# Performance work log

Hardware: AMD Instinct MI355X
Metric: run time of the kernel (lower is better)

The kernel has to match this reference:

```python
import jax, jax.numpy as jnp
import numpy as np

B, T, C = 4, 2048, 1024
N_HEADS = 16
HEAD_DIM = C // N_HEADS


def setup_inputs() -> dict:
    key = jax.random.key(0)
    k1, k2, k3 = jax.random.split(key, 3)
    x = jax.random.normal(k1, (B, T, C), dtype=jnp.float32)
    # torch Linear weights stored as [out, in]; we store as [in, out] for x @ W
    w_qkv = jax.random.normal(k2, (C, 3 * C), dtype=jnp.float32) * (1.0 / np.sqrt(C))
    w_proj = jax.random.normal(k3, (C, C), dtype=jnp.float32) * (1.0 / np.sqrt(C))
    return {"x": x, "w_qkv": w_qkv, "w_proj": w_proj}


def reference(x, w_qkv, w_proj):
    Bx, Tx, Cx = x.shape
    qkv = x @ w_qkv                               # [B,T,3C]
    q, k, v = jnp.split(qkv, 3, axis=-1)

    def to_heads(t):
        return t.reshape(Bx, Tx, N_HEADS, HEAD_DIM).transpose(0, 2, 1, 3)  # [B,H,T,D]

    q, k, v = to_heads(q), to_heads(k), to_heads(v)
    scale = 1.0 / np.sqrt(HEAD_DIM).astype(np.float32)
    scores = jnp.einsum('bhqd,bhkd->bhqk', q, k) * scale  # [B,H,T,T]
    causal = jnp.tril(jnp.ones((Tx, Tx), dtype=bool))
    scores = jnp.where(causal[None, None, :, :], scores, -jnp.inf)
    weights = jax.nn.softmax(scores, axis=-1)
    out = jnp.einsum('bhqk,bhkd->bhqd', weights, v)       # [B,H,T,D]
    out = out.transpose(0, 2, 1, 3).reshape(Bx, Tx, Cx)   # [B,T,C]
    return out @ w_proj
```

## Files before the change

### kernel.cpp

```cpp
#include <hip/hip_runtime.h>
#include <hip/hip_bf16.h>

typedef unsigned short u16;
typedef unsigned int u32;
typedef __attribute__((ext_vector_type(8))) __bf16 bf16x8;
typedef __attribute__((ext_vector_type(4))) float f32x4;
typedef __attribute__((ext_vector_type(4))) short short4v;
typedef __attribute__((ext_vector_type(2))) u32 u32x2;

#define B_ 4
#define T_ 2048
#define C_ 1024
#define NH_ 16
#define HD_ 64

static __device__ __forceinline__ u16 f2bf(float f) {
  u32 u = __builtin_bit_cast(u32, f);
  u32 r = (u + 0x7fffu + ((u >> 16) & 1u)) >> 16;
  return (u16)r;
}

static __device__ __forceinline__ u32 pack2bf(float a, float b) {
  u32 ua = __builtin_bit_cast(u32, a) + 0x8000u;
  u32 ub = __builtin_bit_cast(u32, b) + 0x8000u;
  return __builtin_amdgcn_perm(ub, ua, 0x07060302u);
}

static __device__ __forceinline__ float fexp2(float x) {
#if __has_builtin(__builtin_amdgcn_exp2f)
  return __builtin_amdgcn_exp2f(x);
#else
  return exp2f(x);
#endif
}

static __device__ __forceinline__ void load_lds16(const u16* g, u16* l) {
  __builtin_amdgcn_global_load_lds(
      (const __attribute__((address_space(1))) u32*)g,
      (__attribute__((address_space(3))) u32*)l, 16, 0, 0);
}

static __device__ __forceinline__ f32x4 mfma32(bf16x8 a, bf16x8 b, f32x4 c) {
  return __builtin_amdgcn_mfma_f32_16x16x32_bf16(a, b, c, 0, 0, 0);
}

static __device__ __forceinline__ f32x4 mfma16(short4v a, short4v b, f32x4 c) {
#if __has_builtin(__builtin_amdgcn_mfma_f32_16x16x16bf16_1k)
  return __builtin_amdgcn_mfma_f32_16x16x16bf16_1k(a, b, c, 0, 0, 0);
#else
  asm volatile("v_mfma_f32_16x16x16_bf16 %0, %1, %2, %0\n\t"
               "s_nop 7\n\ts_nop 7"
               : "+v"(c)
               : "v"(a), "v"(b));
  return c;
#endif
}

__global__ __launch_bounds__(256) void cast_bf(const float* __restrict__ in,
                                               u16* __restrict__ out, int n) {
  int i = (blockIdx.x * 256 + threadIdx.x) * 8;
  if (i >= n) return;
  float4 a = *(const float4*)(in + i);
  float4 b = *(const float4*)(in + i + 4);
  u16 r[8] = {f2bf(a.x), f2bf(a.y), f2bf(a.z), f2bf(a.w),
              f2bf(b.x), f2bf(b.y), f2bf(b.z), f2bf(b.w)};
  *(uint4*)(out + i) = *(const uint4*)r;
}

__global__ __launch_bounds__(256) void transpose_cast(const float* __restrict__ in,
                                                      u16* __restrict__ out,
                                                      int K, int N) {
  __shared__ float tile[32][33];
  int bx = blockIdx.x * 32;
  int by = blockIdx.y * 32;
  int tx = threadIdx.x & 31, ty = threadIdx.x >> 5;
  for (int r = ty; r < 32; r += 8)
    tile[r][tx] = in[(size_t)(by + r) * N + bx + tx];
  __syncthreads();
  for (int r = ty; r < 32; r += 8)
    out[(size_t)(bx + r) * K + by + tx] = f2bf(tile[tx][r]);
}

template <bool STORE_BF16, bool SCALE_Q>
__global__ __launch_bounds__(256) void gemm_bt(const u16* __restrict__ A,
                                               const u16* __restrict__ Bt,
                                               void* __restrict__ Cv,
                                               int M, int N, int K,
                                               float qscale) {
  __shared__ __align__(16) u16 As[128 * 64];
  __shared__ __align__(16) u16 Bs[128 * 64];
  const int tid = threadIdx.x;
  const int wave = tid >> 6, lane = tid & 63;
  const int wm = (wave >> 1) * 64, wn = (wave & 1) * 64;
  const int m0 = blockIdx.x * 128, n0 = blockIdx.y * 128;
  const int col = lane & 15, quad = lane >> 4;
  const int lcol = (lane & 7) * 8;
  const int sg = ((lane & 7) ^ ((lane >> 3) & 7)) * 8;
  const int ag = ((quad ^ (col & 7)) * 8);

  f32x4 acc[4][4] = {};

  for (int kt = 0; kt < K; kt += 64) {
    __syncthreads();
    for (int i = 0; i < 4; i++) {
      int row = (wave * 4 + i) * 8 + (lane >> 3);
      load_lds16(A + (size_t)(m0 + row) * K + kt + sg, &As[row * 64 + lcol]);
      load_lds16(Bt + (size_t)(n0 + row) * K + kt + sg, &Bs[row * 64 + lcol]);
    }
    __syncthreads();
    for (int ks = 0; ks < 64; ks += 32) {
      const int o = ag ^ ks;
      bf16x8 af[4], bfr[4];
      for (int t = 0; t < 4; t++) {
        af[t]  = *(const bf16x8*)(&As[(wm + t * 16 + col) * 64 + o]);
        bfr[t] = *(const bf16x8*)(&Bs[(wn + t * 16 + col) * 64 + o]);
      }
      for (int i = 0; i < 4; i++)
        for (int j = 0; j < 4; j++)
          acc[i][j] = mfma32(af[i], bfr[j], acc[i][j]);
    }
  }

  const int rbase = quad * 4;
  for (int i = 0; i < 4; i++)
    for (int j = 0; j < 4; j++) {
      int r = m0 + wm + i * 16 + rbase;
      int c = n0 + wn + j * 16 + col;
      float sc = (SCALE_Q && c < 1024) ? qscale : 1.0f;
      if (STORE_BF16) {
        for (int reg = 0; reg < 4; reg++)
          ((u16*)Cv)[(size_t)(r + reg) * N + c] = f2bf(acc[i][j][reg] * sc);
      } else {
        for (int reg = 0; reg < 4; reg++)
          ((float*)Cv)[(size_t)(r + reg) * N + c] = acc[i][j][reg];
      }
    }
}

__global__ __launch_bounds__(256) void v_permute(const u16* __restrict__ qkv,
                                                 u16* __restrict__ vt) {
  const int jt = blockIdx.x, bh = blockIdx.y, b = bh >> 4, h = bh & 15;
  __shared__ u16 tile[64][68];
  const int tid = threadIdx.x;
  {
    int tl = tid >> 2, c = (tid & 3) * 16;
    const u16* src = qkv + (size_t)(b * 2048 + jt * 64 + tl) * 3072 + 2048 + h * 64 + c;
    *(uint4*)(&tile[tl][c])     = *(const uint4*)(src);
    *(uint4*)(&tile[tl][c + 8]) = *(const uint4*)(src + 8);
  }
  __syncthreads();
  int d = tid >> 2, gq = tid & 3;
  u16 ob[16] __attribute__((aligned(16)));
  for (int j = 0; j < 16; j++) {
    int g = gq * 16 + j;
    int tl = (g & 3) | (((g >> 4) & 3) << 2) | (((g >> 2) & 3) << 4);
    ob[j] = tile[tl][d];
  }
  u16* dst = vt + ((size_t)bh * 64 + d) * 2048 + jt * 64 + gq * 16;
  *(uint4*)(dst) = *(const uint4*)ob;
  *(uint4*)(dst + 8) = *(const uint4*)(ob + 8);
}

__global__ __launch_bounds__(256, 4) void attn_fused(const u16* __restrict__ qkv,
                                                     const u16* __restrict__ vt,
                                                     u16* __restrict__ o) {
  const int i = blockIdx.x >> 6;
  const int bh = blockIdx.x & 63, b = bh >> 4, h = bh & 15;
  const int tid = threadIdx.x, wave = tid >> 6, lane = tid & 63;
  const int col = lane & 15, quad = lane >> 4;

  const int qt0 = i, qt1 = 31 - i;
  const int jtmax = qt1;

  __shared__ __align__(16) u16 Ks[2][4096];
  __shared__ __align__(16) u16 Vs[2][4096];

  const u16* qkb = qkv + (size_t)b * 2048 * 3072;
  const u16* vtb = vt + (size_t)bh * 64 * 2048;

  bf16x8 qf[2][2];
  for (int t = 0; t < 2; t++) {
    int q = (t ? qt1 : qt0) * 64 + wave * 16 + col;
    const u16* qp = qkb + (size_t)q * 3072 + h * 64;
    qf[t][0] = *(const bf16x8*)(qp + quad * 8);
    qf[t][1] = *(const bf16x8*)(qp + 32 + quad * 8);
  }

  f32x4 lacc[2] = {};
  f32x4 Oacc[2][4] = {};

  const int sg  = ((lane & 7) ^ ((lane >> 3) & 7)) * 8;
  const int swq = col & 7;
  const int kg0 = (quad ^ swq) * 8;
  const int vg0 = ((2 * quad) ^ swq) * 8;

  auto stage = [&](int jt, int buf) {
    for (int ii = 0; ii < 2; ii++) {
      int idx = (ii * 4 + wave) * 64 + lane;
      int r = idx >> 3;
      load_lds16(qkb + (size_t)(jt * 64 + r) * 3072 + 1024 + h * 64 + sg,
                 &Ks[buf][idx * 8]);
      load_lds16(vtb + (size_t)r * 2048 + jt * 64 + sg, &Vs[buf][idx * 8]);
    }
  };

  auto softmax_tile = [&](f32x4* s, int t, u32* pbt) {
    f32x4 ps = {};
    for (int nt = 0; nt < 4; nt++) {
      f32x4 p;
      for (int r = 0; r < 4; r++) p[r] = fexp2(s[nt][r]);
      ps += p;
      pbt[nt * 2]     = pack2bf(p[0], p[1]);
      pbt[nt * 2 + 1] = pack2bf(p[2], p[3]);
    }
    lacc[t] += ps;
  };

  stage(0, 0);
  for (int jt = 0; jt <= jtmax; jt++) {
    const int cur = jt & 1;
    __syncthreads();
    if (jt < jtmax) stage(jt + 1, cur ^ 1);

    const u16* K_ = Ks[cur];
    const u16* V_ = Vs[cur];
    const bool act0 = (jt <= qt0);

    f32x4 s0[4] = {}, s1[4] = {};
    for (int nt = 0; nt < 4; nt++) {
      bf16x8 k0 = *(const bf16x8*)(K_ + (nt * 16 + col) * 64 + kg0);
      bf16x8 k1 = *(const bf16x8*)(K_ + (nt * 16 + col) * 64 + (kg0 ^ 32));
      if (act0) {
        s0[nt] = mfma32(k0, qf[0][0], s0[nt]);
        s0[nt] = mfma32(k1, qf[0][1], s0[nt]);
      }
      s1[nt] = mfma32(k0, qf[1][0], s1[nt]);
      s1[nt] = mfma32(k1, qf[1][1], s1[nt]);
    }

    u32 pb0[8], pb1[8];
    if (act0) {
      if (jt == qt0) {
        for (int nt = 0; nt < 4; nt++)
          for (int r = 0; r < 4; r++) {
            int j = nt * 16 + quad * 4 + r, q = wave * 16 + col;
            if (j > q) s0[nt][r] = -INFINITY;
          }
      }
      softmax_tile(s0, 0, pb0);
    }
    if (jt == qt1) {
      for (int nt = 0; nt < 4; nt++)
        for (int r = 0; r < 4; r++) {
          int j = nt * 16 + quad * 4 + r, q = wave * 16 + col;
          if (j > q) s1[nt][r] = -INFINITY;
        }
    }
    softmax_tile(s1, 1, pb1);

    for (int dt = 0; dt < 4; dt++) {
      uint4 vb0 = *(const uint4*)(V_ + (dt * 16 + col) * 64 + vg0);
      uint4 vb1 = *(const uint4*)(V_ + (dt * 16 + col) * 64 + (vg0 ^ 8));
      short4v vf[4];
      vf[0] = __builtin_bit_cast(short4v, (u32x2){vb0.x, vb0.y});
      vf[1] = __builtin_bit_cast(short4v, (u32x2){vb0.z, vb0.w});
      vf[2] = __builtin_bit_cast(short4v, (u32x2){vb1.x, vb1.y});
      vf[3] = __builtin_bit_cast(short4v, (u32x2){vb1.z, vb1.w});
      for (int nt = 0; nt < 4; nt++) {
        if (act0) {
          short4v pf0 = __builtin_bit_cast(short4v, (u32x2){pb0[nt * 2], pb0[nt * 2 + 1]});
          Oacc[0][dt] = mfma16(vf[nt], pf0, Oacc[0][dt]);
        }
        short4v pf1 = __builtin_bit_cast(short4v, (u32x2){pb1[nt * 2], pb1[nt * 2 + 1]});
        Oacc[1][dt] = mfma16(vf[nt], pf1, Oacc[1][dt]);
      }
    }
  }

  for (int t = 0; t < 2; t++) {
    float l = (lacc[t][0] + lacc[t][1]) + (lacc[t][2] + lacc[t][3]);
    l += __shfl_xor(l, 16, 64);
    l += __shfl_xor(l, 32, 64);
    float rl = 1.0f / l;
    int q = (t ? qt1 : qt0) * 64 + wave * 16 + col;
    u16* op = o + (size_t)(b * 2048 + q) * 1024 + h * 64;
    for (int dt = 0; dt < 4; dt++) {
      u16 ob[4] __attribute__((aligned(8)));
      for (int r = 0; r < 4; r++) ob[r] = f2bf(Oacc[t][dt][r] * rl);
      *(uint2*)(op + dt * 16 + quad * 4) = *(const uint2*)ob;
    }
  }
}

extern "C" void kernel_launch(void* const* d_in, const int* in_sizes, int n_in,
                              void* d_out, int out_size, void* d_ws, size_t ws_size,
                              hipStream_t stream) {
  const float* x      = (const float*)d_in[0];
  const float* w_qkv  = (const float*)d_in[1];
  const float* w_proj = (const float*)d_in[2];
  float* out = (float*)d_out;

  u16* x_bf    = (u16*)d_ws;
  u16* wqkvT   = x_bf + (size_t)8192 * 1024;
  u16* wprojT  = wqkvT + (size_t)3072 * 1024;
  u16* qkv_bf  = wprojT + (size_t)1024 * 1024;
  u16* attn_bf = qkv_bf + (size_t)8192 * 3072;
  u16* vt_perm = x_bf;

  const float qscale = 0.125f * 1.44269504f;

  cast_bf<<<4096, 256, 0, stream>>>(x, x_bf, 8192 * 1024);
  transpose_cast<<<dim3(96, 32), 256, 0, stream>>>(w_qkv, wqkvT, 1024, 3072);
  transpose_cast<<<dim3(32, 32), 256, 0, stream>>>(w_proj, wprojT, 1024, 1024);

  gemm_bt<true, true><<<dim3(64, 24), 256, 0, stream>>>(
      x_bf, wqkvT, qkv_bf, 8192, 3072, 1024, qscale);

  v_permute<<<dim3(32, 64), 256, 0, stream>>>(qkv_bf, vt_perm);

  attn_fused<<<1024, 256, 0, stream>>>(qkv_bf, vt_perm, attn_bf);

  gemm_bt<false, false><<<dim3(64, 8), 256, 0, stream>>>(
      attn_bf, wprojT, out, 8192, 1024, 1024, 1.0f);
}
```

Before: 264.6 us.

## Fuse V transpose into QKV GEMM epilogue and merge prep kernels

```diff
diff --git a/kernel.cpp b/kernel.cpp
--- a/kernel.cpp
+++ b/kernel.cpp
@@ -4,6 +4,7 @@
 typedef unsigned short u16;
 typedef unsigned int u32;
 typedef __attribute__((ext_vector_type(8))) __bf16 bf16x8;
+typedef __attribute__((ext_vector_type(2))) __bf16 bf16x2;
 typedef __attribute__((ext_vector_type(4))) float f32x4;
 typedef __attribute__((ext_vector_type(4))) short short4v;
 typedef __attribute__((ext_vector_type(2))) u32 u32x2;
@@ -20,10 +21,15 @@
   return (u16)r;
 }
 
-static __device__ __forceinline__ u32 pack2bf(float a, float b) {
+static __device__ __forceinline__ u32 pk_bf16(float a, float b) {
+#if __has_builtin(__builtin_amdgcn_cvt_pk_bf16_f32)
+  bf16x2 v = __builtin_amdgcn_cvt_pk_bf16_f32(a, b);
+  return __builtin_bit_cast(u32, v);
+#else
   u32 ua = __builtin_bit_cast(u32, a) + 0x8000u;
   u32 ub = __builtin_bit_cast(u32, b) + 0x8000u;
   return __builtin_amdgcn_perm(ub, ua, 0x07060302u);
+#endif
 }
 
 static __device__ __forceinline__ float fexp2(float x) {
@@ -56,24 +62,36 @@
 #endif
 }
 
-__global__ __launch_bounds__(256) void cast_bf(const float* __restrict__ in,
-                                               u16* __restrict__ out, int n) {
-  int i = (blockIdx.x * 256 + threadIdx.x) * 8;
-  if (i >= n) return;
-  float4 a = *(const float4*)(in + i);
-  float4 b = *(const float4*)(in + i + 4);
-  u16 r[8] = {f2bf(a.x), f2bf(a.y), f2bf(a.z), f2bf(a.w),
-              f2bf(b.x), f2bf(b.y), f2bf(b.z), f2bf(b.w)};
-  *(uint4*)(out + i) = *(const uint4*)r;
-}
-
-__global__ __launch_bounds__(256) void transpose_cast(const float* __restrict__ in,
-                                                      u16* __restrict__ out,
-                                                      int K, int N) {
+__global__ __launch_bounds__(256) void prep(const float* __restrict__ x,
+                                            const float* __restrict__ wqkv,
+                                            const float* __restrict__ wproj,
+                                            u16* __restrict__ x_bf,
+                                            u16* __restrict__ wqkvT,
+                                            u16* __restrict__ wprojT) {
   __shared__ float tile[32][33];
-  int bx = blockIdx.x * 32;
-  int by = blockIdx.y * 32;
-  int tx = threadIdx.x & 31, ty = threadIdx.x >> 5;
+  const int bid = blockIdx.x, tid = threadIdx.x;
+  if (bid < 4096) {
+    int i = (bid * 256 + tid) * 8;
+    float4 a = *(const float4*)(x + i);
+    float4 b = *(const float4*)(x + i + 4);
+    u16 r[8] = {f2bf(a.x), f2bf(a.y), f2bf(a.z), f2bf(a.w),
+                f2bf(b.x), f2bf(b.y), f2bf(b.z), f2bf(b.w)};
+    *(uint4*)(x_bf + i) = *(const uint4*)r;
+    return;
+  }
+  const float* in;
+  u16* out;
+  int K = 1024, N, bx, by;
+  if (bid < 4096 + 3072) {
+    int id = bid - 4096;
+    in = wqkv; out = wqkvT; N = 3072;
+    bx = (id % 96) * 32; by = (id / 96) * 32;
+  } else {
+    int id = bid - 7168;
+    in = wproj; out = wprojT; N = 1024;
+    bx = (id % 32) * 32; by = (id / 32) * 32;
+  }
+  int tx = tid & 31, ty = tid >> 5;
   for (int r = ty; r < 32; r += 8)
     tile[r][tx] = in[(size_t)(by + r) * N + bx + tx];
   __syncthreads();
@@ -81,12 +99,84 @@
     out[(size_t)(bx + r) * K + by + tx] = f2bf(tile[tx][r]);
 }
 
-template <bool STORE_BF16, bool SCALE_Q>
-__global__ __launch_bounds__(256) void gemm_bt(const u16* __restrict__ A,
-                                               const u16* __restrict__ Bt,
-                                               void* __restrict__ Cv,
-                                               int M, int N, int K,
-                                               float qscale) {
+__global__ __launch_bounds__(256) void gemm_qkv(const u16* __restrict__ A,
+                                                const u16* __restrict__ Bt,
+                                                u16* __restrict__ qk,
+                                                u16* __restrict__ vt,
+                                                float qscale) {
+  const int K_ = 1024;
+  __shared__ __align__(16) u16 smem[128 * 136];
+  u16* As = smem;
+  u16* Bs = smem + 128 * 64;
+  const int tid = threadIdx.x;
+  const int wave = tid >> 6, lane = tid & 63;
+  const int wm = (wave >> 1) * 64, wn = (wave & 1) * 64;
+  const int m0 = blockIdx.x * 128, n0 = blockIdx.y * 128;
+  const int col = lane & 15, quad = lane >> 4;
+  const int lcol = (lane & 7) * 8;
+  const int sg = ((lane & 7) ^ ((lane >> 3) & 7)) * 8;
+  const int ag = ((quad ^ (col & 7)) * 8);
+
+  f32x4 acc[4][4] = {};
+
+  for (int kt = 0; kt < K_; kt += 64) {
+    __syncthreads();
+    for (int i = 0; i < 4; i++) {
+      int row = (wave * 4 + i) * 8 + (lane >> 3);
+      load_lds16(A + (size_t)(m0 + row) * K_ + kt + sg, &As[row * 64 + lcol]);
+      load_lds16(Bt + (size_t)(n0 + row) * K_ + kt + sg, &Bs[row * 64 + lcol]);
+    }
+    __syncthreads();
+    for (int ks = 0; ks < 64; ks += 32) {
+      const int o = ag ^ ks;
+      bf16x8 af[4], bfr[4];
+      for (int t = 0; t < 4; t++) {
+        af[t]  = *(const bf16x8*)(&As[(wm + t * 16 + col) * 64 + o]);
+        bfr[t] = *(const bf16x8*)(&Bs[(wn + t * 16 + col) * 64 + o]);
+      }
+      for (int i = 0; i < 4; i++)
+        for (int j = 0; j < 4; j++)
+          acc[i][j] = mfma32(af[i], bfr[j], acc[i][j]);
+    }
+  }
+
+  if (n0 < 2048) {
+    for (int i = 0; i < 4; i++)
+      for (int j = 0; j < 4; j++) {
+        int r = m0 + wm + i * 16 + quad * 4;
+        int c = n0 + wn + j * 16 + col;
+        float sc = (c < 1024) ? qscale : 1.0f;
+        for (int reg = 0; reg < 4; reg++)
+          qk[(size_t)(r + reg) * 2048 + c] = f2bf(acc[i][j][reg] * sc);
+      }
+    return;
+  }
+
+  __syncthreads();
+  for (int i = 0; i < 4; i++)
+    for (int j = 0; j < 4; j++) {
+      int cl = wn + j * 16 + col;
+      u16 tmp[4] __attribute__((aligned(8)));
+      for (int reg = 0; reg < 4; reg++) tmp[reg] = f2bf(acc[i][j][reg]);
+      *(unsigned long long*)(&smem[cl * 136 + wm + i * 4 + quad * 16]) =
+          *(const unsigned long long*)tmp;
+    }
+  __syncthreads();
+  {
+    int cl = tid >> 1, half = tid & 1;
+    int cv = (n0 - 2048) + cl, hh = cv >> 6, d = cv & 63;
+    int b = m0 >> 11;
+    u16* dst = vt + ((size_t)((b << 4) + hh) * 64 + d) * 2048 + (m0 & 2047) + half * 64;
+    const u16* src = &smem[cl * 136 + half * 64];
+    for (int ii = 0; ii < 8; ii++)
+      *(uint4*)(dst + ii * 8) = *(const uint4*)(src + ii * 8);
+  }
+}
+
+__global__ __launch_bounds__(256) void gemm_proj(const u16* __restrict__ A,
+                                                 const u16* __restrict__ Bt,
+                                                 float* __restrict__ C,
+                                                 int M, int N, int K) {
   __shared__ __align__(16) u16 As[128 * 64];
   __shared__ __align__(16) u16 Bs[128 * 64];
   const int tid = threadIdx.x;
@@ -121,47 +211,16 @@
     }
   }
 
-  const int rbase = quad * 4;
   for (int i = 0; i < 4; i++)
     for (int j = 0; j < 4; j++) {
-      int r = m0 + wm + i * 16 + rbase;
+      int r = m0 + wm + i * 16 + quad * 4;
       int c = n0 + wn + j * 16 + col;
-      float sc = (SCALE_Q && c < 1024) ? qscale : 1.0f;
-      if (STORE_BF16) {
-        for (int reg = 0; reg < 4; reg++)
-          ((u16*)Cv)[(size_t)(r + reg) * N + c] = f2bf(acc[i][j][reg] * sc);
-      } else {
-        for (int reg = 0; reg < 4; reg++)
-          ((float*)Cv)[(size_t)(r + reg) * N + c] = acc[i][j][reg];
-      }
-    }
-}
-
-__global__ __launch_bounds__(256) void v_permute(const u16* __restrict__ qkv,
-                                                 u16* __restrict__ vt) {
-  const int jt = blockIdx.x, bh = blockIdx.y, b = bh >> 4, h = bh & 15;
-  __shared__ u16 tile[64][68];
-  const int tid = threadIdx.x;
-  {
-    int tl = tid >> 2, c = (tid & 3) * 16;
-    const u16* src = qkv + (size_t)(b * 2048 + jt * 64 + tl) * 3072 + 2048 + h * 64 + c;
-    *(uint4*)(&tile[tl][c])     = *(const uint4*)(src);
-    *(uint4*)(&tile[tl][c + 8]) = *(const uint4*)(src + 8);
-  }
-  __syncthreads();
-  int d = tid >> 2, gq = tid & 3;
-  u16 ob[16] __attribute__((aligned(16)));
-  for (int j = 0; j < 16; j++) {
-    int g = gq * 16 + j;
-    int tl = (g & 3) | (((g >> 4) & 3) << 2) | (((g >> 2) & 3) << 4);
-    ob[j] = tile[tl][d];
-  }
-  u16* dst = vt + ((size_t)bh * 64 + d) * 2048 + jt * 64 + gq * 16;
-  *(uint4*)(dst) = *(const uint4*)ob;
-  *(uint4*)(dst + 8) = *(const uint4*)(ob + 8);
-}
-
-__global__ __launch_bounds__(256, 4) void attn_fused(const u16* __restrict__ qkv,
+      for (int reg = 0; reg < 4; reg++)
+        C[(size_t)(r + reg) * N + c] = acc[i][j][reg];
+    }
+}
+
+__global__ __launch_bounds__(256, 4) void attn_fused(const u16* __restrict__ qk,
                                                      const u16* __restrict__ vt,
                                                      u16* __restrict__ o) {
   const int i = blockIdx.x >> 6;
@@ -175,13 +234,13 @@
   __shared__ __align__(16) u16 Ks[2][4096];
   __shared__ __align__(16) u16 Vs[2][4096];
 
-  const u16* qkb = qkv + (size_t)b * 2048 * 3072;
+  const u16* qkb = qk + (size_t)b * 2048 * 2048;
   const u16* vtb = vt + (size_t)bh * 64 * 2048;
 
   bf16x8 qf[2][2];
   for (int t = 0; t < 2; t++) {
     int q = (t ? qt1 : qt0) * 64 + wave * 16 + col;
-    const u16* qp = qkb + (size_t)q * 3072 + h * 64;
+    const u16* qp = qkb + (size_t)q * 2048 + h * 64;
     qf[t][0] = *(const bf16x8*)(qp + quad * 8);
     qf[t][1] = *(const bf16x8*)(qp + 32 + quad * 8);
   }
@@ -194,14 +253,25 @@
   const int kg0 = (quad ^ swq) * 8;
   const int vg0 = ((2 * quad) ^ swq) * 8;
 
-  auto stage = [&](int jt, int buf) {
-    for (int ii = 0; ii < 2; ii++) {
-      int idx = (ii * 4 + wave) * 64 + lane;
-      int r = idx >> 3;
-      load_lds16(qkb + (size_t)(jt * 64 + r) * 3072 + 1024 + h * 64 + sg,
-                 &Ks[buf][idx * 8]);
-      load_lds16(vtb + (size_t)r * 2048 + jt * 64 + sg, &Vs[buf][idx * 8]);
-    }
+  const int r0 = wave * 8 + (lane >> 3);
+  const int r1 = r0 + 32;
+  const u16* kp0 = qkb + (size_t)r0 * 2048 + 1024 + h * 64 + sg;
+  const u16* kp1 = qkb + (size_t)r1 * 2048 + 1024 + h * 64 + sg;
+  const u16* vp0 = vtb + (size_t)r0 * 2048 + sg;
+  const u16* vp1 = vtb + (size_t)r1 * 2048 + sg;
+  u16* kd0 = &Ks[0][(wave * 64 + lane) * 8];
+  u16* kd1 = kd0 + 2048;
+  u16* vd0 = &Vs[0][(wave * 64 + lane) * 8];
+  u16* vd1 = vd0 + 2048;
+
+  auto stage = [&](int buf) {
+    int bo = buf * 4096;
+    load_lds16(kp0, kd0 + bo);
+    load_lds16(kp1, kd1 + bo);
+    load_lds16(vp0, vd0 + bo);
+    load_lds16(vp1, vd1 + bo);
+    kp0 += 64 * 2048; kp1 += 64 * 2048;
+    vp0 += 64; vp1 += 64;
   };
 
   auto softmax_tile = [&](f32x4* s, int t, u32* pbt) {
@@ -210,17 +280,17 @@
       f32x4 p;
       for (int r = 0; r < 4; r++) p[r] = fexp2(s[nt][r]);
       ps += p;
-      pbt[nt * 2]     = pack2bf(p[0], p[1]);
-      pbt[nt * 2 + 1] = pack2bf(p[2], p[3]);
+      pbt[nt * 2]     = pk_bf16(p[0], p[1]);
+      pbt[nt * 2 + 1] = pk_bf16(p[2], p[3]);
     }
     lacc[t] += ps;
   };
 
-  stage(0, 0);
+  stage(0);
   for (int jt = 0; jt <= jtmax; jt++) {
     const int cur = jt & 1;
     __syncthreads();
-    if (jt < jtmax) stage(jt + 1, cur ^ 1);
+    if (jt < jtmax) stage(cur ^ 1);
 
     const u16* K_ = Ks[cur];
     const u16* V_ = Vs[cur];
@@ -303,23 +373,17 @@
   u16* x_bf    = (u16*)d_ws;
   u16* wqkvT   = x_bf + (size_t)8192 * 1024;
   u16* wprojT  = wqkvT + (size_t)3072 * 1024;
-  u16* qkv_bf  = wprojT + (size_t)1024 * 1024;
-  u16* attn_bf = qkv_bf + (size_t)8192 * 3072;
-  u16* vt_perm = x_bf;
+  u16* qk_buf  = wprojT + (size_t)1024 * 1024;
+  u16* vt_perm = qk_buf + (size_t)8192 * 2048;
+  u16* attn_bf = vt_perm + (size_t)64 * 64 * 2048;
 
   const float qscale = 0.125f * 1.44269504f;
 
-  cast_bf<<<4096, 256, 0, stream>>>(x, x_bf, 8192 * 1024);
-  transpose_cast<<<dim3(96, 32), 256, 0, stream>>>(w_qkv, wqkvT, 1024, 3072);
-  transpose_cast<<<dim3(32, 32), 256, 0, stream>>>(w_proj, wprojT, 1024, 1024);
-
-  gemm_bt<true, true><<<dim3(64, 24), 256, 0, stream>>>(
-      x_bf, wqkvT, qkv_bf, 8192, 3072, 1024, qscale);
-
-  v_permute<<<dim3(32, 64), 256, 0, stream>>>(qkv_bf, vt_perm);
-
-  attn_fused<<<1024, 256, 0, stream>>>(qkv_bf, vt_perm, attn_bf);
-
-  gemm_bt<false, false><<<dim3(64, 8), 256, 0, stream>>>(
-      attn_bf, wprojT, out, 8192, 1024, 1024, 1.0f);
-}
+  prep<<<8192, 256, 0, stream>>>(x, w_qkv, w_proj, x_bf, wqkvT, wprojT);
+
+  gemm_qkv<<<dim3(64, 24), 256, 0, stream>>>(x_bf, wqkvT, qk_buf, vt_perm, qscale);
+
+  attn_fused<<<1024, 256, 0, stream>>>(qk_buf, vt_perm, attn_bf);
+
+  gemm_proj<<<dim3(64, 8), 256, 0, stream>>>(attn_bf, wprojT, out, 8192, 1024, 1024);
+}
```

New measurement: 243.4 us. -8.0%, faster.
